# Optimization experiments

Measured on AMD Instinct MI355X. Metric: run time of the kernel, lower is better.

The kernel has to match this reference:

```python
import jax, jax.numpy as jnp
import numpy as np

D_MODEL = 1024
ATT_MODEL = 1024
NHEAD = 16
HEAD_DIM = ATT_MODEL // NHEAD
B, S = 2, 2048


def setup_inputs() -> dict:
    key = jax.random.key(0)
    ks = jax.random.split(key, 5)
    sc = 1.0 / np.sqrt(D_MODEL)
    return {
        "x": jax.random.normal(ks[0], (B, S, D_MODEL), dtype=jnp.float32),
        "Wq": jax.random.normal(ks[1], (D_MODEL, ATT_MODEL), dtype=jnp.float32) * sc,
        "bq": jnp.zeros((ATT_MODEL,), dtype=jnp.float32),
        "Wk": jax.random.normal(ks[2], (D_MODEL, ATT_MODEL), dtype=jnp.float32) * sc,
        "bk": jnp.zeros((ATT_MODEL,), dtype=jnp.float32),
        "Wv": jax.random.normal(ks[3], (D_MODEL, ATT_MODEL), dtype=jnp.float32) * sc,
        "bv": jnp.zeros((ATT_MODEL,), dtype=jnp.float32),
        "Wo": jax.random.normal(ks[4], (ATT_MODEL, D_MODEL), dtype=jnp.float32) * sc,
        "bo": jnp.zeros((D_MODEL,), dtype=jnp.float32),
    }


def reference(x, Wq, bq, Wk, bk, Wv, bv, Wo, bo):
    b, s, _ = x.shape
    # projections [B,S,att_model] -> [B,H,S,Dh]
    def split_heads(t):
        return t.reshape(b, s, NHEAD, HEAD_DIM).transpose(0, 2, 1, 3)
    Q = split_heads(x @ Wq + bq)
    K = split_heads(x @ Wk + bk)
    V = split_heads(x @ Wv + bv)
    # dk = sqrt(att_model / nhead) = sqrt(head_dim)
    dk = jnp.asarray(HEAD_DIM, x.dtype) ** 0.5
    scores = jnp.einsum("bhqd,bhkd->bhqk", Q, K) / dk  # [B,H,S,S]
    attn = jax.nn.softmax(scores, axis=-1)
    out = jnp.einsum("bhqk,bhkd->bhqd", attn, V)       # [B,H,S,Dh]
    out = out.transpose(0, 2, 1, 3).reshape(b, s, ATT_MODEL)
    return out @ Wo + bo
```

## Files before the change

kernel.cpp:

```cpp
#include <hip/hip_runtime.h>
#include <hip/hip_bf16.h>
#include <math.h>

#define D_MODEL 1024
#define ATT 1024
#define NHEAD 16
#define HDIM 64
#define BATCH 2
#define SEQ 2048
#define M_ROWS (BATCH * SEQ)

typedef unsigned short u16;
typedef unsigned int u32;
typedef __bf16 bf16x8 __attribute__((ext_vector_type(8)));
typedef float f4 __attribute__((ext_vector_type(4)));
typedef u16 u16x8 __attribute__((ext_vector_type(8)));
typedef u16 u16x4 __attribute__((ext_vector_type(4)));

static_assert(sizeof(u16x8) == 16, "u16x8 must be 16B");

__device__ __forceinline__ u16 f32_to_bf16(float f) {
    union { float f; unsigned u; } c; c.f = f;
    unsigned u = c.u;
    return (u16)((u + 0x7FFFu + ((u >> 16) & 1u)) >> 16);
}
__device__ __forceinline__ float bf16_to_f32(u16 h) {
    union { unsigned u; float f; } c; c.u = ((unsigned)h) << 16;
    return c.f;
}
__device__ __forceinline__ void split2(float f, u16& hi, u16& lo) {
    hi = f32_to_bf16(f);
    lo = f32_to_bf16(f - bf16_to_f32(hi));
}

__device__ __forceinline__ f4 mfma16(u16x8 a, u16x8 b, f4 c) {
    union U { u16x8 u; bf16x8 b; };
    U ua, ub; ua.u = a; ub.u = b;
    return __builtin_amdgcn_mfma_f32_16x16x32_bf16(ua.b, ub.b, c, 0, 0, 0);
}

__device__ __forceinline__ void gload16(const void* g, void* l) {
    __builtin_amdgcn_global_load_lds(
        (const __attribute__((address_space(1))) void*)g,
        (__attribute__((address_space(3))) void*)l, 16, 0, 0);
}

template <int N>
__device__ __forceinline__ void waitcnt_vm() {
    if constexpr (N == 0)      asm volatile("s_waitcnt vmcnt(0)" ::: "memory");
    else if constexpr (N == 4) asm volatile("s_waitcnt vmcnt(4)" ::: "memory");
    else if constexpr (N == 6) asm volatile("s_waitcnt vmcnt(6)" ::: "memory");
    else if constexpr (N == 8) asm volatile("s_waitcnt vmcnt(8)" ::: "memory");
}
#define BARRIER() __builtin_amdgcn_s_barrier()

__global__ __launch_bounds__(256) void k_split(const float* __restrict__ in,
                                               u16* __restrict__ hi,
                                               u16* __restrict__ lo, int n4) {
    int i = blockIdx.x * blockDim.x + threadIdx.x;
    if (i >= n4) return;
    const float4 v = ((const float4*)in)[i];
    float vv[4] = {v.x, v.y, v.z, v.w};
    u16 hh[4], ll[4];
#pragma unroll
    for (int j = 0; j < 4; ++j) split2(vv[j], hh[j], ll[j]);
    u16x4 hv = {hh[0], hh[1], hh[2], hh[3]};
    u16x4 lv = {ll[0], ll[1], ll[2], ll[3]};
    *(u16x4*)(hi + (size_t)i * 4) = hv;
    *(u16x4*)(lo + (size_t)i * 4) = lv;
}

__global__ __launch_bounds__(256) void k_splitT(const float* __restrict__ W,
                                                u16* __restrict__ hiT,
                                                u16* __restrict__ loT) {
    __shared__ float tile[32][33];
    int n0 = blockIdx.x * 32, k0 = blockIdx.y * 32;
    int tx = threadIdx.x, ty = threadIdx.y;
#pragma unroll
    for (int j = 0; j < 4; ++j) {
        int r = ty + j * 8;
        tile[r][tx] = W[(size_t)(k0 + r) * ATT + n0 + tx];
    }
    __syncthreads();
#pragma unroll
    for (int j = 0; j < 4; ++j) {
        int r = ty + j * 8;
        float v = tile[tx][r];
        u16 h, l; split2(v, h, l);
        hiT[(size_t)(n0 + r) * D_MODEL + k0 + tx] = h;
        loT[(size_t)(n0 + r) * D_MODEL + k0 + tx] = l;
    }
}

__global__ __launch_bounds__(256) void k_transpose(
    const u16* __restrict__ src_h, const u16* __restrict__ src_l,
    u16* __restrict__ dst_h, u16* __restrict__ dst_l, int srcld, int dstld) {
    __shared__ u16 t[64][72];
    const u16* src = blockIdx.z ? src_l : src_h;
    u16* dst = blockIdx.z ? dst_l : dst_h;
    int n0 = blockIdx.x * 64, m0 = blockIdx.y * 64;
    int tid = threadIdx.x;
    int r = tid >> 2, c16 = (tid & 3) * 16;
    *(u16x8*)&t[r][c16]     = *(const u16x8*)&src[(size_t)(m0 + r) * srcld + n0 + c16];
    *(u16x8*)&t[r][c16 + 8] = *(const u16x8*)&src[(size_t)(m0 + r) * srcld + n0 + c16 + 8];
    __syncthreads();
    u16x8 o0, o1;
#pragma unroll
    for (int j = 0; j < 8; ++j) { o0[j] = t[c16 + j][r]; o1[j] = t[c16 + 8 + j][r]; }
    *(u16x8*)&dst[(size_t)(n0 + r) * dstld + m0 + c16]     = o0;
    *(u16x8*)&dst[(size_t)(n0 + r) * dstld + m0 + c16 + 8] = o1;
}

template <int MF, int SPLIT_OUT>
__global__ __launch_bounds__(256) void k_gemm(
    const u16* __restrict__ Ah, const u16* __restrict__ Al,
    const u16* __restrict__ Bh, const u16* __restrict__ Bl,
    const float* __restrict__ bq, const float* __restrict__ bk,
    const float* __restrict__ bv,
    float* __restrict__ Co, u16* __restrict__ Ch, u16* __restrict__ Cl,
    int M, int N, int K, int NBX) {
    constexpr int BM = MF * 32;
    constexpr int SAe = BM * 32;
    constexpr int NCH = (2 * BM + 256) / 16;
    constexpr int CPW = NCH / 4;
    constexpr int BUFE = (2 * BM + 256) * 32;
    __shared__ u16 sh[2 * BUFE];

    int tid = threadIdx.x;
    int wave = tid >> 6, lane = tid & 63, lg = lane >> 4, ln = lane & 15;
    int wm = wave >> 1, wn = wave & 1;

    int nb = gridDim.x;
    int bs = (blockIdx.x & 7) * (nb >> 3) + (blockIdx.x >> 3);
    int bx = bs % NBX, by = bs / NBX;
    int m0 = by * BM, n0 = bx * 128;

    f4 acc[MF][4];
#pragma unroll
    for (int i = 0; i < MF; ++i)
#pragma unroll
        for (int j = 0; j < 4; ++j) acc[i][j] = f4{0.f, 0.f, 0.f, 0.f};

    const u16* gp[CPW];
#pragma unroll
    for (int j = 0; j < CPW; ++j) {
        int c = wave * CPW + j;
        int bo = c << 10;
        const u16* base; int local, r0;
        if (bo < BM * 64)                { base = Ah; local = bo;                 r0 = m0; }
        else if (bo < 2 * BM * 64)       { base = Al; local = bo - BM * 64;       r0 = m0; }
        else if (bo < 2 * BM * 64 + 8192){ base = Bh; local = bo - 2 * BM * 64;   r0 = n0; }
        else                             { base = Bl; local = bo - 2 * BM * 64 - 8192; r0 = n0; }
        int lo2 = local + lane * 16;
        int row = lo2 >> 6;
        int cb  = (lo2 >> 4) & 3;
        int cbs = cb ^ ((row >> 1) & 3);
        gp[j] = base + (size_t)(r0 + row) * K + cbs * 8;
    }

    int offA[MF], offB[4];
#pragma unroll
    for (int mf = 0; mf < MF; ++mf) {
        int row = wm * (MF * 16) + mf * 16 + ln;
        offA[mf] = row * 32 + ((lg ^ ((row >> 1) & 3)) << 3);
    }
#pragma unroll
    for (int nf = 0; nf < 4; ++nf) {
        int row = wn * 64 + nf * 16 + ln;
        offB[nf] = row * 32 + ((lg ^ ((row >> 1) & 3)) << 3);
    }

    auto stage = [&](int bsel) {
#pragma unroll
        for (int j = 0; j < CPW; ++j)
            gload16(gp[j], (char*)sh + bsel * (BUFE * 2) + ((wave * CPW + j) << 10));
    };
    auto adv = [&]() {
#pragma unroll
        for (int j = 0; j < CPW; ++j) gp[j] += 32;
    };
    auto compute = [&](int sb) {
        u16x8 a_h[MF], a_l[MF], b_h[4], b_l[4];
#pragma unroll
        for (int mf = 0; mf < MF; ++mf) {
            a_h[mf] = *(const u16x8*)&sh[sb + offA[mf]];
            a_l[mf] = *(const u16x8*)&sh[sb + SAe + offA[mf]];
        }
#pragma unroll
        for (int nf = 0; nf < 4; ++nf) {
            b_h[nf] = *(const u16x8*)&sh[sb + 2 * SAe + offB[nf]];
            b_l[nf] = *(const u16x8*)&sh[sb + 2 * SAe + 4096 + offB[nf]];
        }
#pragma unroll
        for (int mf = 0; mf < MF; ++mf)
#pragma unroll
            for (int nf = 0; nf < 4; ++nf) {
                acc[mf][nf] = mfma16(a_h[mf], b_h[nf], acc[mf][nf]);
                acc[mf][nf] = mfma16(a_h[mf], b_l[nf], acc[mf][nf]);
                acc[mf][nf] = mfma16(a_l[mf], b_h[nf], acc[mf][nf]);
            }
    };

    const int NS = K / 32;
    stage(0); adv();
    for (int t = 0; t < NS - 2; t += 2) {
        stage(1); adv();
        waitcnt_vm<CPW>(); BARRIER();
        compute(0);
        BARRIER();
        stage(0); adv();
        waitcnt_vm<CPW>(); BARRIER();
        compute(BUFE);
        BARRIER();
    }
    stage(1);
    waitcnt_vm<CPW>(); BARRIER();
    compute(0);
    BARRIER();
    waitcnt_vm<0>(); BARRIER();
    compute(BUFE);

#pragma unroll
    for (int mf = 0; mf < MF; ++mf)
#pragma unroll
        for (int nf = 0; nf < 4; ++nf) {
            int col = n0 + wn * 64 + nf * 16 + ln;
            float bb;
            if (bk) bb = col < 1024 ? bq[col] : (col < 2048 ? bk[col - 1024] : bv[col - 2048]);
            else    bb = bq[col];
#pragma unroll
            for (int r = 0; r < 4; ++r) {
                int row = m0 + wm * (MF * 16) + mf * 16 + lg * 4 + r;
                float v = acc[mf][nf][r] + bb;
                if (SPLIT_OUT) {
                    u16 h, l; split2(v, h, l);
                    Ch[(size_t)row * N + col] = h;
                    Cl[(size_t)row * N + col] = l;
                } else {
                    Co[(size_t)row * N + col] = v;
                }
            }
        }
}

#define ATTN_SCALE 0.18033688f

__global__ __launch_bounds__(512, 1) void k_attn(
    const u16* __restrict__ qkv_h, const u16* __restrict__ qkv_l,
    const u16* __restrict__ vt_h, const u16* __restrict__ vt_l,
    u16* __restrict__ Oh, u16* __restrict__ Ol) {
    __shared__ u16 sh[49152];
    int tid = threadIdx.x;
    int w = tid >> 6, lane = tid & 63, lg = lane >> 4, ln = lane & 15;

    int bs = (blockIdx.x & 7) * 32 + (blockIdx.x >> 3);
    int qt = bs & 7, h = (bs >> 3) & 15, b = bs >> 7;
    int q0 = qt * 256;

    u16x8 qh[2][2], ql[2][2];
#pragma unroll
    for (int mf = 0; mf < 2; ++mf) {
        int row = q0 + w * 32 + mf * 16 + ln;
        const u16* ph_ = qkv_h + (size_t)(b * SEQ + row) * 3072 + h * HDIM;
        const u16* pl_ = qkv_l + (size_t)(b * SEQ + row) * 3072 + h * HDIM;
#pragma unroll
        for (int ks = 0; ks < 2; ++ks) {
            qh[mf][ks] = *(const u16x8*)(ph_ + ks * 32 + lg * 8);
            ql[mf][ks] = *(const u16x8*)(pl_ + ks * 32 + lg * 8);
        }
    }

    f4 acco[2][4], accl[2];
#pragma unroll
    for (int i = 0; i < 2; ++i) {
#pragma unroll
        for (int j = 0; j < 4; ++j) acco[i][j] = f4{0.f, 0.f, 0.f, 0.f};
        accl[i] = f4{0.f, 0.f, 0.f, 0.f};
    }
    float run_m[2][4];
#pragma unroll
    for (int i = 0; i < 2; ++i)
#pragma unroll
        for (int r = 0; r < 4; ++r) run_m[i][r] = -INFINITY;

    u16x8 ones;
#pragma unroll
    for (int j = 0; j < 8; ++j) ones[j] = 0x3F80;

    int bt = w >> 1, hf = w & 1;
    const u16* gp[4];
    {
        int row0 = hf * 32 + (lane >> 3);
        int kbs = (lane & 7) ^ (lane >> 3);
        const u16* base;
        if (bt == 0)      base = qkv_h + (size_t)(b * SEQ) * 3072 + 1024 + h * HDIM;
        else if (bt == 1) base = qkv_l + (size_t)(b * SEQ) * 3072 + 1024 + h * HDIM;
        else if (bt == 2) base = vt_h + (size_t)(h * HDIM) * M_ROWS + b * SEQ;
        else              base = vt_l + (size_t)(h * HDIM) * M_ROWS + b * SEQ;
        size_t rs = (bt < 2) ? 3072 : M_ROWS;
#pragma unroll
        for (int j = 0; j < 4; ++j)
            gp[j] = base + (size_t)(row0 + j * 8) * rs + kbs * 8;
    }
    const int gstride = (bt < 2) ? 64 * 3072 : 64;
    const int sbase = bt * 8192 + hf * 4096;

    auto stage = [&](int bsel) {
#pragma unroll
        for (int j = 0; j < 4; ++j)
            gload16(gp[j], (char*)sh + sbase + (j << 10) + bsel * 32768);
    };
    auto adv = [&]() {
#pragma unroll
        for (int j = 0; j < 4; ++j) gp[j] += gstride;
    };

    int offQK[4][2], offPr[2][2];
#pragma unroll
    for (int nf = 0; nf < 4; ++nf) {
        int krow = nf * 16 + ln;
#pragma unroll
        for (int ks = 0; ks < 2; ++ks)
            offQK[nf][ks] = krow * 64 + (((4 * ks + lg) ^ (krow & 7)) << 3);
    }
#pragma unroll
    for (int mf = 0; mf < 2; ++mf) {
        int prow = w * 32 + mf * 16 + ln;
#pragma unroll
        for (int ks = 0; ks < 2; ++ks)
            offPr[mf][ks] = 32768 + prow * 64 + (((4 * ks + lg) ^ (prow & 7)) << 3);
    }

    auto compute = [&](int base) {
        f4 s[2][4];
#pragma unroll
        for (int i = 0; i < 2; ++i)
#pragma unroll
            for (int j = 0; j < 4; ++j) s[i][j] = f4{0.f, 0.f, 0.f, 0.f};
#pragma unroll
        for (int nf = 0; nf < 4; ++nf) {
#pragma unroll
            for (int ks = 0; ks < 2; ++ks) {
                u16x8 bh = *(const u16x8*)&sh[base + offQK[nf][ks]];
                u16x8 bl = *(const u16x8*)&sh[base + 4096 + offQK[nf][ks]];
#pragma unroll
                for (int mf = 0; mf < 2; ++mf) {
                    s[mf][nf] = mfma16(qh[mf][ks], bh, s[mf][nf]);
                    s[mf][nf] = mfma16(qh[mf][ks], bl, s[mf][nf]);
                    s[mf][nf] = mfma16(ql[mf][ks], bh, s[mf][nf]);
                }
            }
        }
#pragma unroll
        for (int mf = 0; mf < 2; ++mf) {
#pragma unroll
            for (int r = 0; r < 4; ++r) {
                float mx = fmaxf(fmaxf(s[mf][0][r], s[mf][1][r]),
                                 fmaxf(s[mf][2][r], s[mf][3][r]));
#pragma unroll
                for (int d = 1; d < 16; d <<= 1) mx = fmaxf(mx, __shfl_xor(mx, d));
                float mx2 = mx * ATTN_SCALE;
                bool need = mx2 > run_m[mf][r] + 11.0f;
                float nm = need ? mx2 : run_m[mf][r];
                int qrow = w * 32 + mf * 16 + lg * 4 + r;
                int swz = qrow & 7;
                int pbase = 32768 + qrow * 64 + (ln & 7);
#pragma unroll
                for (int nf = 0; nf < 4; ++nf) {
                    float p = __builtin_amdgcn_exp2f(s[mf][nf][r] * ATTN_SCALE - nm);
                    sh[pbase + (((nf * 2 + (ln >> 3)) ^ swz) << 3)] = f32_to_bf16(p);
                }
                if (__any((int)need)) {
                    float corr = __builtin_amdgcn_exp2f(run_m[mf][r] - nm);
#pragma unroll
                    for (int nf = 0; nf < 4; ++nf) acco[mf][nf][r] *= corr;
                    accl[mf][r] *= corr;
                    run_m[mf][r] = nm;
                }
            }
        }
#pragma unroll
        for (int ks = 0; ks < 2; ++ks) {
            u16x8 pa[2];
#pragma unroll
            for (int mf = 0; mf < 2; ++mf)
                pa[mf] = *(const u16x8*)&sh[offPr[mf][ks]];
#pragma unroll
            for (int nf = 0; nf < 4; ++nf) {
                u16x8 vh = *(const u16x8*)&sh[base + 8192 + offQK[nf][ks]];
                u16x8 vl = *(const u16x8*)&sh[base + 12288 + offQK[nf][ks]];
#pragma unroll
                for (int mf = 0; mf < 2; ++mf) {
                    acco[mf][nf] = mfma16(pa[mf], vh, acco[mf][nf]);
                    acco[mf][nf] = mfma16(pa[mf], vl, acco[mf][nf]);
                }
            }
            accl[0] = mfma16(pa[0], ones, accl[0]);
            accl[1] = mfma16(pa[1], ones, accl[1]);
        }
    };

    stage(0); adv();
    for (int t = 0; t < 30; t += 2) {
        stage(1); adv();
        waitcnt_vm<4>(); BARRIER();
        compute(0);
        BARRIER();
        stage(0); adv();
        waitcnt_vm<4>(); BARRIER();
        compute(16384);
        BARRIER();
    }
    stage(1);
    waitcnt_vm<4>(); BARRIER();
    compute(0);
    BARRIER();
    waitcnt_vm<0>(); BARRIER();
    compute(16384);

#pragma unroll
    for (int mf = 0; mf < 2; ++mf)
#pragma unroll
        for (int nf = 0; nf < 4; ++nf) {
            int col = h * HDIM + nf * 16 + ln;
#pragma unroll
            for (int r = 0; r < 4; ++r) {
                int row = q0 + w * 32 + mf * 16 + lg * 4 + r;
                float v = acco[mf][nf][r] / accl[mf][r];
                u16 hh, ll; split2(v, hh, ll);
                Oh[(size_t)(b * SEQ + row) * ATT + col] = hh;
                Ol[(size_t)(b * SEQ + row) * ATT + col] = ll;
            }
        }
}

extern "C" void kernel_launch(void* const* d_in, const int* in_sizes, int n_in,
                              void* d_out, int out_size, void* d_ws, size_t ws_size,
                              hipStream_t stream) {
    const float* x  = (const float*)d_in[0];
    const float* Wq = (const float*)d_in[1];
    const float* bq = (const float*)d_in[2];
    const float* Wk = (const float*)d_in[3];
    const float* bk = (const float*)d_in[4];
    const float* Wv = (const float*)d_in[5];
    const float* bv = (const float*)d_in[6];
    const float* Wo = (const float*)d_in[7];
    const float* bo = (const float*)d_in[8];
    float* out = (float*)d_out;

    const size_t MK = (size_t)M_ROWS * ATT;
    const size_t WE = (size_t)D_MODEL * ATT;
    const size_t M3 = (size_t)M_ROWS * 3072;

    char* p = (char*)d_ws;
    auto alloc = [&](size_t bytes) -> u16* {
        u16* r = (u16*)p;
        p += (bytes + 255) & ~(size_t)255;
        return r;
    };
    u16* x_hi  = alloc(MK * 2); u16* x_lo  = alloc(MK * 2);
    u16* wT_h  = alloc(3 * WE * 2); u16* wT_l  = alloc(3 * WE * 2);
    u16* woT_h = alloc(WE * 2); u16* woT_l = alloc(WE * 2);
    u16* qkv_h = alloc(M3 * 2); u16* qkv_l = alloc(M3 * 2);
    u16* vt_h  = alloc(MK * 2); u16* vt_l  = alloc(MK * 2);
    u16* at_h = x_hi; u16* at_l = x_lo;

    k_split<<<dim3((unsigned)(MK / 4 / 256)), 256, 0, stream>>>(x, x_hi, x_lo, (int)(MK / 4));

    dim3 bt(32, 8), gt(32, 32);
    k_splitT<<<gt, bt, 0, stream>>>(Wq, wT_h, wT_l);
    k_splitT<<<gt, bt, 0, stream>>>(Wk, wT_h + WE, wT_l + WE);
    k_splitT<<<gt, bt, 0, stream>>>(Wv, wT_h + 2 * WE, wT_l + 2 * WE);
    k_splitT<<<gt, bt, 0, stream>>>(Wo, woT_h, woT_l);

    k_gemm<4, 1><<<768, 256, 0, stream>>>(x_hi, x_lo, wT_h, wT_l, bq, bk, bv,
                                          nullptr, qkv_h, qkv_l, M_ROWS, 3072, 1024, 24);

    k_transpose<<<dim3(16, 64, 2), 256, 0, stream>>>(qkv_h + 2048, qkv_l + 2048,
                                                     vt_h, vt_l, 3072, M_ROWS);

    k_attn<<<256, 512, 0, stream>>>(qkv_h, qkv_l, vt_h, vt_l, at_h, at_l);

    k_gemm<2, 0><<<512, 256, 0, stream>>>(at_h, at_l, woT_h, woT_l, bo, nullptr, nullptr,
                                          out, nullptr, nullptr, M_ROWS, 1024, 1024, 8);
}
```

Baseline: 331.0 us.

## Drop low-precision K and V terms in attention, shrink attention blocks

Attention now keeps only the high bf16 part of K and V. The Q·K product falls from three MFMAs to two (qh·kh and ql·kh) and P·V from two to one. The QKV GEMM no longer writes the low halves for the K and V columns, and the V transpose handles only the high part. The attention kernel is reshaped to 256-thread blocks over 128-query tiles with half the shared memory, so more blocks can be resident. Accuracy drops because the K and V low-order corrections are gone.

```diff
diff --git a/kernel.cpp b/kernel.cpp
--- a/kernel.cpp
+++ b/kernel.cpp
@@ -235,7 +235,7 @@
                 if (SPLIT_OUT) {
                     u16 h, l; split2(v, h, l);
                     Ch[(size_t)row * N + col] = h;
-                    Cl[(size_t)row * N + col] = l;
+                    if (col < 1024) Cl[(size_t)row * N + col] = l;
                 } else {
                     Co[(size_t)row * N + col] = v;
                 }
@@ -245,17 +245,17 @@
 
 #define ATTN_SCALE 0.18033688f
 
-__global__ __launch_bounds__(512, 1) void k_attn(
+__global__ __launch_bounds__(256) void k_attn(
     const u16* __restrict__ qkv_h, const u16* __restrict__ qkv_l,
-    const u16* __restrict__ vt_h, const u16* __restrict__ vt_l,
+    const u16* __restrict__ vt,
     u16* __restrict__ Oh, u16* __restrict__ Ol) {
-    __shared__ u16 sh[49152];
+    __shared__ u16 sh[24576];
     int tid = threadIdx.x;
     int w = tid >> 6, lane = tid & 63, lg = lane >> 4, ln = lane & 15;
 
-    int bs = (blockIdx.x & 7) * 32 + (blockIdx.x >> 3);
-    int qt = bs & 7, h = (bs >> 3) & 15, b = bs >> 7;
-    int q0 = qt * 256;
+    int bs = (blockIdx.x & 7) * 64 + (blockIdx.x >> 3);
+    int qt = bs & 15, h = (bs >> 4) & 15, b = bs >> 8;
+    int q0 = qt * 128;
 
     u16x8 qh[2][2], ql[2][2];
 #pragma unroll
@@ -290,25 +290,27 @@
     int bt = w >> 1, hf = w & 1;
     const u16* gp[4];
     {
-        int row0 = hf * 32 + (lane >> 3);
+        int r0 = hf * 32 + (lane >> 3);
         int kbs = (lane & 7) ^ (lane >> 3);
-        const u16* base;
-        if (bt == 0)      base = qkv_h + (size_t)(b * SEQ) * 3072 + 1024 + h * HDIM;
-        else if (bt == 1) base = qkv_l + (size_t)(b * SEQ) * 3072 + 1024 + h * HDIM;
-        else if (bt == 2) base = vt_h + (size_t)(h * HDIM) * M_ROWS + b * SEQ;
-        else              base = vt_l + (size_t)(h * HDIM) * M_ROWS + b * SEQ;
-        size_t rs = (bt < 2) ? 3072 : M_ROWS;
+        if (bt == 0) {
+            const u16* base = qkv_h + (size_t)(b * SEQ) * 3072 + 1024 + h * HDIM;
+#pragma unroll
+            for (int j = 0; j < 4; ++j)
+                gp[j] = base + (size_t)(r0 + j * 8) * 3072 + kbs * 8;
+        } else {
+            const u16* base = vt + (size_t)(h * HDIM) * M_ROWS + b * SEQ;
+#pragma unroll
+            for (int j = 0; j < 4; ++j)
+                gp[j] = base + (size_t)(r0 + j * 8) * M_ROWS + kbs * 8;
+        }
+    }
+    const int gstride = (bt == 0) ? 64 * 3072 : 64;
+    const int cb0 = (w * 4) << 10;
+
+    auto stage = [&](int bsel) {
 #pragma unroll
         for (int j = 0; j < 4; ++j)
-            gp[j] = base + (size_t)(row0 + j * 8) * rs + kbs * 8;
-    }
-    const int gstride = (bt < 2) ? 64 * 3072 : 64;
-    const int sbase = bt * 8192 + hf * 4096;
-
-    auto stage = [&](int bsel) {
-#pragma unroll
-        for (int j = 0; j < 4; ++j)
-            gload16(gp[j], (char*)sh + sbase + (j << 10) + bsel * 32768);
+            gload16(gp[j], (char*)sh + cb0 + (j << 10) + bsel * 16384);
     };
     auto adv = [&]() {
 #pragma unroll
@@ -328,7 +330,7 @@
         int prow = w * 32 + mf * 16 + ln;
 #pragma unroll
         for (int ks = 0; ks < 2; ++ks)
-            offPr[mf][ks] = 32768 + prow * 64 + (((4 * ks + lg) ^ (prow & 7)) << 3);
+            offPr[mf][ks] = 16384 + prow * 64 + (((4 * ks + lg) ^ (prow & 7)) << 3);
     }
 
     auto compute = [&](int base) {
@@ -342,11 +344,9 @@
 #pragma unroll
             for (int ks = 0; ks < 2; ++ks) {
                 u16x8 bh = *(const u16x8*)&sh[base + offQK[nf][ks]];
-                u16x8 bl = *(const u16x8*)&sh[base + 4096 + offQK[nf][ks]];
 #pragma unroll
                 for (int mf = 0; mf < 2; ++mf) {
                     s[mf][nf] = mfma16(qh[mf][ks], bh, s[mf][nf]);
-                    s[mf][nf] = mfma16(qh[mf][ks], bl, s[mf][nf]);
                     s[mf][nf] = mfma16(ql[mf][ks], bh, s[mf][nf]);
                 }
             }
@@ -364,7 +364,7 @@
                 float nm = need ? mx2 : run_m[mf][r];
                 int qrow = w * 32 + mf * 16 + lg * 4 + r;
                 int swz = qrow & 7;
-                int pbase = 32768 + qrow * 64 + (ln & 7);
+                int pbase = 16384 + qrow * 64 + (ln & 7);
 #pragma unroll
                 for (int nf = 0; nf < 4; ++nf) {
                     float p = __builtin_amdgcn_exp2f(s[mf][nf][r] * ATTN_SCALE - nm);
@@ -387,13 +387,10 @@
                 pa[mf] = *(const u16x8*)&sh[offPr[mf][ks]];
 #pragma unroll
             for (int nf = 0; nf < 4; ++nf) {
-                u16x8 vh = *(const u16x8*)&sh[base + 8192 + offQK[nf][ks]];
-                u16x8 vl = *(const u16x8*)&sh[base + 12288 + offQK[nf][ks]];
-#pragma unroll
-                for (int mf = 0; mf < 2; ++mf) {
+                u16x8 vh = *(const u16x8*)&sh[base + 4096 + offQK[nf][ks]];
+#pragma unroll
+                for (int mf = 0; mf < 2; ++mf)
                     acco[mf][nf] = mfma16(pa[mf], vh, acco[mf][nf]);
-                    acco[mf][nf] = mfma16(pa[mf], vl, acco[mf][nf]);
-                }
             }
             accl[0] = mfma16(pa[0], ones, accl[0]);
             accl[1] = mfma16(pa[1], ones, accl[1]);
@@ -408,7 +405,7 @@
         BARRIER();
         stage(0); adv();
         waitcnt_vm<4>(); BARRIER();
-        compute(16384);
+        compute(8192);
         BARRIER();
     }
     stage(1);
@@ -416,7 +413,7 @@
     compute(0);
     BARRIER();
     waitcnt_vm<0>(); BARRIER();
-    compute(16384);
+    compute(8192);
 
 #pragma unroll
     for (int mf = 0; mf < 2; ++mf)
@@ -476,10 +473,10 @@
     k_gemm<4, 1><<<768, 256, 0, stream>>>(x_hi, x_lo, wT_h, wT_l, bq, bk, bv,
                                           nullptr, qkv_h, qkv_l, M_ROWS, 3072, 1024, 24);
 
-    k_transpose<<<dim3(16, 64, 2), 256, 0, stream>>>(qkv_h + 2048, qkv_l + 2048,
+    k_transpose<<<dim3(16, 64, 1), 256, 0, stream>>>(qkv_h + 2048, qkv_l + 2048,
                                                      vt_h, vt_l, 3072, M_ROWS);
 
-    k_attn<<<256, 512, 0, stream>>>(qkv_h, qkv_l, vt_h, vt_l, at_h, at_l);
+    k_attn<<<512, 256, 0, stream>>>(qkv_h, qkv_l, vt_h, at_h, at_l);
 
     k_gemm<2, 0><<<512, 256, 0, stream>>>(at_h, at_l, woT_h, woT_l, bo, nullptr, nullptr,
                                           out, nullptr, nullptr, M_ROWS, 1024, 1024, 8);
```

New measurement: 315.0 us. 1.05x faster.
